# Kernel tuning notes

Measured on AMD Instinct MI355X. Metric: run time of the kernel, lower is better.

The kernel has to match this reference:

```python
import jax, jax.numpy as jnp
import numpy as np

INPUT_DIM = 512
NUM_CLASSES = 1000


def setup_inputs() -> dict:
    key = jax.random.key(0)
    kx, kw, kb = jax.random.split(key, 3)
    x = jax.random.normal(kx, (16384, INPUT_DIM), dtype=jnp.float32)
    # Stacked per-class Linear(input_dim, 2) params: W [C, 2, D], b [C, 2]
    lim = 1.0 / np.sqrt(INPUT_DIM)
    W = jax.random.uniform(kw, (NUM_CLASSES, 2, INPUT_DIM), dtype=jnp.float32, minval=-lim, maxval=lim)
    b = jax.random.uniform(kb, (NUM_CLASSES, 2), dtype=jnp.float32, minval=-lim, maxval=lim)
    return {"x": x, "W": W, "b": b}


def reference(x, W, b):
    # logits[b, c, t] = x[b, :] @ W[c, t, :] + b[c, t]
    logits = jnp.einsum("bd,ctd->bct", x, W) + b[None, :, :]  # [B, C, 2]
    # LogSoftmax over the 2 logits per class (torch dim=1 of the [B,2] slice)
    return jax.nn.log_softmax(logits, axis=-1)
```

## Files before the change

### kernel.cpp

```cpp
#include <hip/hip_runtime.h>
#include <cstdint>
#include <cstddef>

typedef unsigned short u16;
typedef unsigned int u32;
typedef __bf16 bf16x8 __attribute__((ext_vector_type(8)));
typedef float f32x4 __attribute__((ext_vector_type(4)));
typedef float f32x2 __attribute__((ext_vector_type(2)));
typedef u32 u32x4 __attribute__((ext_vector_type(4)));

#define M_TOT 16384
#define C_TOT 1000
#define N_PAD 1024
#define K_TOT 512
#define OUT_STRIDE 2000
#define BM 128
#define BN 128
#define BK 32
#define NT 16
#define NWG 1024

__device__ __forceinline__ u16 f2bf(float f) {
  u32 u = __float_as_uint(f);
  u = (u + 0x7FFFu + ((u >> 16) & 1u)) >> 16;
  return (u16)u;
}

__device__ __forceinline__ u32 cvtpk(float lo, float hi) {
  u32 d;
  asm("v_cvt_pk_bf16_f32 %0, %1, %2" : "=v"(d) : "v"(lo), "v"(hi));
  return d;
}

__global__ __launch_bounds__(256) void wprep_kernel(const float* __restrict__ W,
                                                    const float* __restrict__ b,
                                                    u16* __restrict__ wd,
                                                    float* __restrict__ bd) {
  const int i = blockIdx.x * 256 + threadIdx.x;
  const int c = i >> 6;
  const int seg = i & 63;
  ushort4 r0 = {0, 0, 0, 0}, r1 = {0, 0, 0, 0};
  if (c < C_TOT) {
    const float4* w0 = (const float4*)(W + (size_t)(2 * c) * K_TOT) + seg * 2;
    const float4* w1 = (const float4*)(W + (size_t)(2 * c + 1) * K_TOT) + seg * 2;
    float4 a0 = w0[0], a1 = w0[1], c0 = w1[0], c1 = w1[1];
    r0.x = f2bf(a0.x - c0.x); r0.y = f2bf(a0.y - c0.y);
    r0.z = f2bf(a0.z - c0.z); r0.w = f2bf(a0.w - c0.w);
    r1.x = f2bf(a1.x - c1.x); r1.y = f2bf(a1.y - c1.y);
    r1.z = f2bf(a1.z - c1.z); r1.w = f2bf(a1.w - c1.w);
    if (seg == 0) bd[c] = b[2 * c] - b[2 * c + 1];
  } else if (seg == 0) {
    bd[c] = 0.0f;
  }
  ushort4* d = (ushort4*)(wd + (size_t)c * K_TOT);
  d[seg * 2] = r0;
  d[seg * 2 + 1] = r1;
}

__device__ __forceinline__ void gload_lds(const u16* g, u16* l) {
  __builtin_amdgcn_global_load_lds((const __attribute__((address_space(1))) u32*)g,
                                   (__attribute__((address_space(3))) u32*)l, 16, 0, 0);
}

__device__ __forceinline__ void stage8k(const u16* __restrict__ gbase,
                                        u16* lb, int tid) {
#pragma unroll
  for (int i = 0; i < 2; ++i) {
    const int g = i * 256 + tid;
    const int lrow = g >> 3;
    const int u = (g & 7) ^ (lrow & 7);
    const int r = lrow | ((u >> 2) << 6);
    const int q = u & 3;
    gload_lds(gbase + (size_t)r * K_TOT + q * 8, lb + (size_t)g * 8);
  }
}

#define VMW(N) asm volatile("s_waitcnt vmcnt(" #N ")" ::: "memory")
#define CFENCE asm volatile("" ::: "memory")

__global__ __launch_bounds__(256, 4) void gemm_ls_kernel(const float* __restrict__ Af,
                                                         const u16* __restrict__ B,
                                                         const float* __restrict__ bdiff,
                                                         float* __restrict__ out) {
  __shared__ u16 As[2][4096];
  __shared__ u16 Bs[3][4096];

  const int tid = threadIdx.x;
  const int lane = tid & 63;
  const int w = tid >> 6;
  const int wm = w >> 1;
  const int wn = w & 1;

  const int bid = blockIdx.x;
  const int wg = (bid & 7) * (NWG / 8) + (bid >> 3);
  const int m0 = (wg >> 3) * BM;
  const int n0 = (wg & 7) * BN;

  const float* gAf = Af + (size_t)m0 * K_TOT;
  const u16* gB = B + (size_t)n0 * K_TOT;

  const int lrow0 = tid >> 3;
  const int au = (tid & 7) ^ (lrow0 & 7);
  const int qA = au & 3;
  const int rA0 = lrow0 | ((au >> 2) << 6);
  const int rA1 = (32 + lrow0) | ((au >> 2) << 6);
  const f32x4* gq0 = (const f32x4*)gAf + (size_t)rA0 * 128 + qA * 2;
  const f32x4* gq1 = (const f32x4*)gAf + (size_t)rA1 * 128 + qA * 2;

  const int ar = lane & 15;
  const int kq4 = lane >> 4;
  int offA[4], offB[4];
#pragma unroll
  for (int i = 0; i < 4; ++i) {
    int r = wm * 64 + i * 16 + ar;
    offA[i] = (r & 63) * 128 + (((((r >> 6) << 2) | kq4) ^ (r & 7)) << 4);
    r = wn * 64 + i * 16 + ar;
    offB[i] = (r & 63) * 128 + (((((r >> 6) << 2) | kq4) ^ (r & 7)) << 4);
  }

  f32x4 acc[4][4] = {};
  f32x4 areg[2][4];

#define ALOAD(T)                                   \
  do {                                             \
    areg[(T) & 1][0] = gq0[(T) * 8];               \
    areg[(T) & 1][1] = gq0[(T) * 8 + 1];           \
    areg[(T) & 1][2] = gq1[(T) * 8];               \
    areg[(T) & 1][3] = gq1[(T) * 8 + 1];           \
  } while (0)

#define ACVT_WR(T)                                                        \
  do {                                                                    \
    u32x4 w0, w1;                                                         \
    w0.x = cvtpk(areg[(T) & 1][0].x, areg[(T) & 1][0].y);                 \
    w0.y = cvtpk(areg[(T) & 1][0].z, areg[(T) & 1][0].w);                 \
    w0.z = cvtpk(areg[(T) & 1][1].x, areg[(T) & 1][1].y);                 \
    w0.w = cvtpk(areg[(T) & 1][1].z, areg[(T) & 1][1].w);                 \
    w1.x = cvtpk(areg[(T) & 1][2].x, areg[(T) & 1][2].y);                 \
    w1.y = cvtpk(areg[(T) & 1][2].z, areg[(T) & 1][2].w);                 \
    w1.z = cvtpk(areg[(T) & 1][3].x, areg[(T) & 1][3].y);                 \
    w1.w = cvtpk(areg[(T) & 1][3].z, areg[(T) & 1][3].w);                 \
    *(u32x4*)(&As[(T) & 1][(size_t)tid * 8]) = w0;                        \
    *(u32x4*)(&As[(T) & 1][(size_t)(256 + tid) * 8]) = w1;                \
  } while (0)

#define BSTAGE(T) stage8k(gB + (T) * BK, &Bs[(T) % 3][0], tid)

#define COMPUTE(T)                                                          \
  do {                                                                      \
    bf16x8 af[4], bf[4];                                                    \
    _Pragma("unroll") for (int i = 0; i < 4; ++i)                           \
        af[i] = *(const bf16x8*)((const char*)&As[(T) & 1][0] + offA[i]);   \
    _Pragma("unroll") for (int i = 0; i < 4; ++i)                           \
        bf[i] = *(const bf16x8*)((const char*)&Bs[(T) % 3][0] + offB[i]);   \
    _Pragma("unroll") for (int mi = 0; mi < 4; ++mi)                        \
        _Pragma("unroll") for (int ni = 0; ni < 4; ++ni)                    \
            acc[mi][ni] = __builtin_amdgcn_mfma_f32_16x16x32_bf16(          \
                af[mi], bf[ni], acc[mi][ni], 0, 0, 0);                      \
  } while (0)

#define STEP(T, VMN)                                         \
  do {                                                       \
    VMW(VMN);                                                \
    CFENCE;                                                  \
    ACVT_WR(T);                                              \
    if ((T) + 1 < NT) ALOAD((T) + 1);                        \
    asm volatile("s_waitcnt lgkmcnt(0)" ::: "memory");       \
    __builtin_amdgcn_s_barrier();                            \
    CFENCE;                                                  \
    if ((T) + 2 < NT) BSTAGE((T) + 2);                       \
    __builtin_amdgcn_s_setprio(1);                           \
    COMPUTE(T);                                              \
    __builtin_amdgcn_s_setprio(0);                           \
  } while (0)

  ALOAD(0);
  CFENCE;
  BSTAGE(0);
  BSTAGE(1);
  CFENCE;

  STEP(0, 2);   STEP(1, 2);   STEP(2, 2);   STEP(3, 2);
  STEP(4, 2);   STEP(5, 2);   STEP(6, 2);   STEP(7, 2);
  STEP(8, 2);   STEP(9, 2);   STEP(10, 2);  STEP(11, 2);
  STEP(12, 2);  STEP(13, 2);  STEP(14, 2);  STEP(15, 0);

  const int rbase = m0 + wm * 64 + (lane >> 4) * 4;
  const bool full = (n0 + BN <= C_TOT);

#pragma unroll
  for (int ni = 0; ni < 4; ++ni) {
    const int n = n0 + wn * 64 + ni * 16 + ar;
    if (full || n < C_TOT) {
      const float bd_r = bdiff[n];
#pragma unroll
      for (int mi = 0; mi < 4; ++mi) {
#pragma unroll
        for (int j = 0; j < 4; ++j) {
          const float d = acc[mi][ni][j] + bd_r;
          const float o0 = fminf(d, 0.0f) - __logf(1.0f + __expf(-fabsf(d)));
          const int row = rbase + mi * 16 + j;
          f32x2 v;
          v.x = o0;
          v.y = o0 - d;
          *(f32x2*)(out + (size_t)row * OUT_STRIDE + 2 * n) = v;
        }
      }
    }
  }
#undef ALOAD
#undef ACVT_WR
#undef BSTAGE
#undef COMPUTE
#undef STEP
}

__global__ __launch_bounds__(256) void naive_kernel(const float* __restrict__ x,
                                                    const float* __restrict__ W,
                                                    const float* __restrict__ b,
                                                    float* __restrict__ out) {
  __shared__ float xs[K_TOT];
  const int row = blockIdx.x;
  for (int i = threadIdx.x; i < K_TOT; i += 256) xs[i] = x[(size_t)row * K_TOT + i];
  __syncthreads();
  for (int c = threadIdx.x; c < C_TOT; c += 256) {
    const float* w0 = W + (size_t)c * 1024;
    float l0 = b[c * 2], l1 = b[c * 2 + 1];
    for (int k = 0; k < K_TOT; ++k) {
      const float xv = xs[k];
      l0 += xv * w0[k];
      l1 += xv * w0[K_TOT + k];
    }
    const float d = l0 - l1;
    const float t = __logf(1.0f + __expf(-fabsf(d)));
    out[(size_t)row * OUT_STRIDE + c * 2]     = fminf(d, 0.0f) - t;
    out[(size_t)row * OUT_STRIDE + c * 2 + 1] = fminf(-d, 0.0f) - t;
  }
}

extern "C" void kernel_launch(void* const* d_in, const int* in_sizes, int n_in,
                              void* d_out, int out_size, void* d_ws, size_t ws_size,
                              hipStream_t stream) {
  const float* x = (const float*)d_in[0];
  const float* W = (const float*)d_in[1];
  const float* b = (const float*)d_in[2];
  float* out = (float*)d_out;

  const size_t nwd = (size_t)N_PAD * K_TOT;
  const size_t need = nwd * sizeof(u16) + N_PAD * sizeof(float);

  if (ws_size < need) {
    naive_kernel<<<M_TOT, 256, 0, stream>>>(x, W, b, out);
    return;
  }

  u16* wd = (u16*)d_ws;
  float* bd = (float*)(wd + nwd);

  wprep_kernel<<<256, 256, 0, stream>>>(W, b, wd, bd);
  gemm_ls_kernel<<<NWG, 256, 0, stream>>>(x, wd, bd, out);
}
```

Before: 48.78 us.

## Process two M tiles per workgroup and overlap first epilogue with second tile's loads

Halves the grid so each workgroup computes two consecutive 128-row tiles against the same B column block. The second tile's A and B prefetches are issued before the first tile's log-softmax epilogue, so the output stores and transcendental math can overlap with global loads. This cuts launch and prologue cost per tile, but halves the number of workgroups, which may reduce occupancy and wave-level parallelism across CUs.

```diff
diff --git a/kernel.cpp b/kernel.cpp
--- a/kernel.cpp
+++ b/kernel.cpp
@@ -18,7 +18,7 @@
 #define BN 128
 #define BK 32
 #define NT 16
-#define NWG 1024
+#define NWG 512
 
 __device__ __forceinline__ u16 f2bf(float f) {
   u32 u = __float_as_uint(f);
@@ -93,10 +93,10 @@
 
   const int bid = blockIdx.x;
   const int wg = (bid & 7) * (NWG / 8) + (bid >> 3);
-  const int m0 = (wg >> 3) * BM;
+  const int m_base = (wg >> 3) * (2 * BM);
   const int n0 = (wg & 7) * BN;
 
-  const float* gAf = Af + (size_t)m0 * K_TOT;
+  const float* gAf = Af + (size_t)m_base * K_TOT;
   const u16* gB = B + (size_t)n0 * K_TOT;
 
   const int lrow0 = tid >> 3;
@@ -120,13 +120,14 @@
 
   f32x4 acc[4][4] = {};
   f32x4 areg[2][4];
-
-#define ALOAD(T)                                   \
-  do {                                             \
-    areg[(T) & 1][0] = gq0[(T) * 8];               \
-    areg[(T) & 1][1] = gq0[(T) * 8 + 1];           \
-    areg[(T) & 1][2] = gq1[(T) * 8];               \
-    areg[(T) & 1][3] = gq1[(T) * 8 + 1];           \
+  const bool full = (n0 + BN <= C_TOT);
+
+#define ALOAD(TOFF, T)                                   \
+  do {                                                   \
+    areg[(T) & 1][0] = gq0[(TOFF) + (T) * 8];            \
+    areg[(T) & 1][1] = gq0[(TOFF) + (T) * 8 + 1];        \
+    areg[(T) & 1][2] = gq1[(TOFF) + (T) * 8];            \
+    areg[(T) & 1][3] = gq1[(TOFF) + (T) * 8 + 1];        \
   } while (0)
 
 #define ACVT_WR(T)                                                        \
@@ -159,12 +160,12 @@
                 af[mi], bf[ni], acc[mi][ni], 0, 0, 0);                      \
   } while (0)
 
-#define STEP(T, VMN)                                         \
+#define STEP(TOFF, T, VMN)                                   \
   do {                                                       \
     VMW(VMN);                                                \
     CFENCE;                                                  \
     ACVT_WR(T);                                              \
-    if ((T) + 1 < NT) ALOAD((T) + 1);                        \
+    if ((T) + 1 < NT) ALOAD(TOFF, (T) + 1);                  \
     asm volatile("s_waitcnt lgkmcnt(0)" ::: "memory");       \
     __builtin_amdgcn_s_barrier();                            \
     CFENCE;                                                  \
@@ -174,45 +175,68 @@
     __builtin_amdgcn_s_setprio(0);                           \
   } while (0)
 
-  ALOAD(0);
+#define EPI(M0V)                                                            \
+  do {                                                                      \
+    const int rbase = (M0V) + wm * 64 + (lane >> 4) * 4;                    \
+    _Pragma("unroll") for (int ni = 0; ni < 4; ++ni) {                      \
+      const int n = n0 + wn * 64 + ni * 16 + ar;                            \
+      if (full || n < C_TOT) {                                              \
+        const float bd_r = bdiff[n];                                        \
+        _Pragma("unroll") for (int mi = 0; mi < 4; ++mi) {                  \
+          _Pragma("unroll") for (int j = 0; j < 4; ++j) {                   \
+            const float d = acc[mi][ni][j] + bd_r;                          \
+            const float o0 = fminf(d, 0.0f) - __logf(1.0f + __expf(-fabsf(d))); \
+            const int row = rbase + mi * 16 + j;                            \
+            f32x2 v;                                                        \
+            v.x = o0;                                                       \
+            v.y = o0 - d;                                                   \
+            *(f32x2*)(out + (size_t)row * OUT_STRIDE + 2 * n) = v;          \
+          }                                                                 \
+        }                                                                   \
+      }                                                                     \
+    }                                                                       \
+  } while (0)
+
+  ALOAD(0, 0);
   CFENCE;
   BSTAGE(0);
   BSTAGE(1);
   CFENCE;
 
-  STEP(0, 2);   STEP(1, 2);   STEP(2, 2);   STEP(3, 2);
-  STEP(4, 2);   STEP(5, 2);   STEP(6, 2);   STEP(7, 2);
-  STEP(8, 2);   STEP(9, 2);   STEP(10, 2);  STEP(11, 2);
-  STEP(12, 2);  STEP(13, 2);  STEP(14, 2);  STEP(15, 0);
-
-  const int rbase = m0 + wm * 64 + (lane >> 4) * 4;
-  const bool full = (n0 + BN <= C_TOT);
-
-#pragma unroll
-  for (int ni = 0; ni < 4; ++ni) {
-    const int n = n0 + wn * 64 + ni * 16 + ar;
-    if (full || n < C_TOT) {
-      const float bd_r = bdiff[n];
-#pragma unroll
-      for (int mi = 0; mi < 4; ++mi) {
-#pragma unroll
-        for (int j = 0; j < 4; ++j) {
-          const float d = acc[mi][ni][j] + bd_r;
-          const float o0 = fminf(d, 0.0f) - __logf(1.0f + __expf(-fabsf(d)));
-          const int row = rbase + mi * 16 + j;
-          f32x2 v;
-          v.x = o0;
-          v.y = o0 - d;
-          *(f32x2*)(out + (size_t)row * OUT_STRIDE + 2 * n) = v;
-        }
-      }
-    }
-  }
+  STEP(0, 0, 2);   STEP(0, 1, 2);   STEP(0, 2, 2);   STEP(0, 3, 2);
+  STEP(0, 4, 2);   STEP(0, 5, 2);   STEP(0, 6, 2);   STEP(0, 7, 2);
+  STEP(0, 8, 2);   STEP(0, 9, 2);   STEP(0, 10, 2);  STEP(0, 11, 2);
+  STEP(0, 12, 2);  STEP(0, 13, 2);  STEP(0, 14, 2);  STEP(0, 15, 0);
+
+  __builtin_amdgcn_s_barrier();
+  CFENCE;
+  ALOAD(16384, 0);
+  BSTAGE(0);
+  BSTAGE(1);
+  CFENCE;
+  EPI(m_base);
+  CFENCE;
+
+#pragma unroll
+  for (int mi = 0; mi < 4; ++mi)
+#pragma unroll
+    for (int ni = 0; ni < 4; ++ni)
+#pragma unroll
+      for (int j = 0; j < 4; ++j) acc[mi][ni][j] = 0.0f;
+
+  STEP(16384, 0, 2);   STEP(16384, 1, 2);   STEP(16384, 2, 2);   STEP(16384, 3, 2);
+  STEP(16384, 4, 2);   STEP(16384, 5, 2);   STEP(16384, 6, 2);   STEP(16384, 7, 2);
+  STEP(16384, 8, 2);   STEP(16384, 9, 2);   STEP(16384, 10, 2);  STEP(16384, 11, 2);
+  STEP(16384, 12, 2);  STEP(16384, 13, 2);  STEP(16384, 14, 2);  STEP(16384, 15, 0);
+
+  EPI(m_base + BM);
+
 #undef ALOAD
 #undef ACVT_WR
 #undef BSTAGE
 #undef COMPUTE
 #undef STEP
+#undef EPI
 }
 
 __global__ __launch_bounds__(256) void naive_kernel(const float* __restrict__ x,
```

Result: slower. 77.77 us (+59.4%).

## Process two M tiles per block and overlap first tile's epilogue with second GEMM

Applied to the files above, without the earlier changes.

Halves BN to 64 and has each workgroup compute two consecutive 128-row M tiles. The first tile's biased logits are packed to bf16 in registers and their log-softmax stores are interleaved into the second tile's main loop, hiding output-write latency behind MFMA work. This cuts accumulator registers per tile, but it reduces B reuse per A load and rounds the first tile's logits to bf16 before the epilogue, which lowers output precision.

```diff
diff --git a/kernel.cpp b/kernel.cpp
--- a/kernel.cpp
+++ b/kernel.cpp
@@ -15,7 +15,7 @@
 #define K_TOT 512
 #define OUT_STRIDE 2000
 #define BM 128
-#define BN 128
+#define BN 64
 #define BK 32
 #define NT 16
 #define NWG 1024
@@ -62,17 +62,11 @@
                                    (__attribute__((address_space(3))) u32*)l, 16, 0, 0);
 }
 
-__device__ __forceinline__ void stage8k(const u16* __restrict__ gbase,
+__device__ __forceinline__ void stage4k(const u16* __restrict__ gbase,
                                         u16* lb, int tid) {
-#pragma unroll
-  for (int i = 0; i < 2; ++i) {
-    const int g = i * 256 + tid;
-    const int lrow = g >> 3;
-    const int u = (g & 7) ^ (lrow & 7);
-    const int r = lrow | ((u >> 2) << 6);
-    const int q = u & 3;
-    gload_lds(gbase + (size_t)r * K_TOT + q * 8, lb + (size_t)g * 8);
-  }
+  const int r = tid >> 2;
+  const int q = (tid & 3) ^ (r & 3);
+  gload_lds(gbase + (size_t)r * K_TOT + q * 8, lb + (size_t)tid * 8);
 }
 
 #define VMW(N) asm volatile("s_waitcnt vmcnt(" #N ")" ::: "memory")
@@ -83,7 +77,7 @@
                                                          const float* __restrict__ bdiff,
                                                          float* __restrict__ out) {
   __shared__ u16 As[2][4096];
-  __shared__ u16 Bs[3][4096];
+  __shared__ u16 Bs[3][2048];
 
   const int tid = threadIdx.x;
   const int lane = tid & 63;
@@ -93,10 +87,10 @@
 
   const int bid = blockIdx.x;
   const int wg = (bid & 7) * (NWG / 8) + (bid >> 3);
-  const int m0 = (wg >> 3) * BM;
-  const int n0 = (wg & 7) * BN;
-
-  const float* gAf = Af + (size_t)m0 * K_TOT;
+  const int m_base = (wg >> 4) * (2 * BM);
+  const int n0 = (wg & 15) * BN;
+
+  const float* gAf = Af + (size_t)m_base * K_TOT;
   const u16* gB = B + (size_t)n0 * K_TOT;
 
   const int lrow0 = tid >> 3;
@@ -109,24 +103,32 @@
 
   const int ar = lane & 15;
   const int kq4 = lane >> 4;
-  int offA[4], offB[4];
+  int offA[4], offB[2];
 #pragma unroll
   for (int i = 0; i < 4; ++i) {
-    int r = wm * 64 + i * 16 + ar;
+    const int r = wm * 64 + i * 16 + ar;
     offA[i] = (r & 63) * 128 + (((((r >> 6) << 2) | kq4) ^ (r & 7)) << 4);
-    r = wn * 64 + i * 16 + ar;
-    offB[i] = (r & 63) * 128 + (((((r >> 6) << 2) | kq4) ^ (r & 7)) << 4);
-  }
-
-  f32x4 acc[4][4] = {};
+  }
+#pragma unroll
+  for (int i = 0; i < 2; ++i) {
+    const int r = wn * 32 + i * 16 + ar;
+    offB[i] = r * 64 + ((kq4 ^ (r & 3)) << 4);
+  }
+
+  const bool full = (n0 + BN <= C_TOT);
+  const float bd0 = bdiff[n0 + wn * 32 + ar];
+  const float bd1 = bdiff[n0 + wn * 32 + 16 + ar];
+  CFENCE;
+
+  f32x4 acc[4][2] = {};
   f32x4 areg[2][4];
 
-#define ALOAD(T)                                   \
-  do {                                             \
-    areg[(T) & 1][0] = gq0[(T) * 8];               \
-    areg[(T) & 1][1] = gq0[(T) * 8 + 1];           \
-    areg[(T) & 1][2] = gq1[(T) * 8];               \
-    areg[(T) & 1][3] = gq1[(T) * 8 + 1];           \
+#define ALOAD(TOFF, T)                                   \
+  do {                                                   \
+    areg[(T) & 1][0] = gq0[(TOFF) + (T) * 8];            \
+    areg[(T) & 1][1] = gq0[(TOFF) + (T) * 8 + 1];        \
+    areg[(T) & 1][2] = gq1[(TOFF) + (T) * 8];            \
+    areg[(T) & 1][3] = gq1[(TOFF) + (T) * 8 + 1];        \
   } while (0)
 
 #define ACVT_WR(T)                                                        \
@@ -144,27 +146,43 @@
     *(u32x4*)(&As[(T) & 1][(size_t)(256 + tid) * 8]) = w1;                \
   } while (0)
 
-#define BSTAGE(T) stage8k(gB + (T) * BK, &Bs[(T) % 3][0], tid)
+#define BSTAGE(T) stage4k(gB + (T) * BK, &Bs[(T) % 3][0], tid)
 
 #define COMPUTE(T)                                                          \
   do {                                                                      \
-    bf16x8 af[4], bf[4];                                                    \
+    bf16x8 af[4], bf[2];                                                    \
     _Pragma("unroll") for (int i = 0; i < 4; ++i)                           \
         af[i] = *(const bf16x8*)((const char*)&As[(T) & 1][0] + offA[i]);   \
-    _Pragma("unroll") for (int i = 0; i < 4; ++i)                           \
+    _Pragma("unroll") for (int i = 0; i < 2; ++i)                           \
         bf[i] = *(const bf16x8*)((const char*)&Bs[(T) % 3][0] + offB[i]);   \
     _Pragma("unroll") for (int mi = 0; mi < 4; ++mi)                        \
-        _Pragma("unroll") for (int ni = 0; ni < 4; ++ni)                    \
+        _Pragma("unroll") for (int ni = 0; ni < 2; ++ni)                    \
             acc[mi][ni] = __builtin_amdgcn_mfma_f32_16x16x32_bf16(          \
                 af[mi], bf[ni], acc[mi][ni], 0, 0, 0);                      \
   } while (0)
 
-#define STEP(T, VMN)                                         \
+#define STONE(K)                                                            \
+  do {                                                                      \
+    const int ni_ = (K) >> 4, mi_ = ((K) >> 2) & 3, j_ = (K) & 3;           \
+    const int n_ = n0 + wn * 32 + ni_ * 16 + ar;                            \
+    if (full || n_ < C_TOT) {                                               \
+      const u32 w_ = dsv[ni_ * 8 + mi_ * 2 + (j_ >> 1)];                    \
+      const float d_ = __uint_as_float((j_ & 1) ? (w_ & 0xffff0000u) : (w_ << 16)); \
+      const float o0 = fminf(d_, 0.0f) - __logf(1.0f + __expf(-fabsf(d_))); \
+      const int row = m_base + wm * 64 + mi_ * 16 + (lane >> 4) * 4 + j_;   \
+      f32x2 v_;                                                             \
+      v_.x = o0;                                                            \
+      v_.y = o0 - d_;                                                       \
+      *(f32x2*)(out + (size_t)row * OUT_STRIDE + 2 * n_) = v_;              \
+    }                                                                       \
+  } while (0)
+
+#define STEP0(T, VMN)                                        \
   do {                                                       \
     VMW(VMN);                                                \
     CFENCE;                                                  \
     ACVT_WR(T);                                              \
-    if ((T) + 1 < NT) ALOAD((T) + 1);                        \
+    if ((T) + 1 < NT) ALOAD(0, (T) + 1);                     \
     asm volatile("s_waitcnt lgkmcnt(0)" ::: "memory");       \
     __builtin_amdgcn_s_barrier();                            \
     CFENCE;                                                  \
@@ -174,32 +192,79 @@
     __builtin_amdgcn_s_setprio(0);                           \
   } while (0)
 
-  ALOAD(0);
+#define STEP1(T, VMN)                                        \
+  do {                                                       \
+    VMW(VMN);                                                \
+    CFENCE;                                                  \
+    ACVT_WR(T);                                              \
+    if ((T) + 1 < NT) ALOAD(16384, (T) + 1);                 \
+    asm volatile("s_waitcnt lgkmcnt(0)" ::: "memory");       \
+    __builtin_amdgcn_s_barrier();                            \
+    CFENCE;                                                  \
+    if ((T) + 2 < NT) BSTAGE((T) + 2);                       \
+    STONE(2 * (T));                                          \
+    STONE(2 * (T) + 1);                                      \
+    __builtin_amdgcn_s_setprio(1);                           \
+    COMPUTE(T);                                              \
+    __builtin_amdgcn_s_setprio(0);                           \
+  } while (0)
+
+  ALOAD(0, 0);
   CFENCE;
   BSTAGE(0);
   BSTAGE(1);
   CFENCE;
 
-  STEP(0, 2);   STEP(1, 2);   STEP(2, 2);   STEP(3, 2);
-  STEP(4, 2);   STEP(5, 2);   STEP(6, 2);   STEP(7, 2);
-  STEP(8, 2);   STEP(9, 2);   STEP(10, 2);  STEP(11, 2);
-  STEP(12, 2);  STEP(13, 2);  STEP(14, 2);  STEP(15, 0);
-
-  const int rbase = m0 + wm * 64 + (lane >> 4) * 4;
-  const bool full = (n0 + BN <= C_TOT);
-
-#pragma unroll
-  for (int ni = 0; ni < 4; ++ni) {
-    const int n = n0 + wn * 64 + ni * 16 + ar;
+  STEP0(0, 1);   STEP0(1, 1);   STEP0(2, 1);   STEP0(3, 1);
+  STEP0(4, 1);   STEP0(5, 1);   STEP0(6, 1);   STEP0(7, 1);
+  STEP0(8, 1);   STEP0(9, 1);   STEP0(10, 1);  STEP0(11, 1);
+  STEP0(12, 1);  STEP0(13, 1);  STEP0(14, 1);  STEP0(15, 0);
+
+  u32 dsv[16];
+#pragma unroll
+  for (int ni = 0; ni < 2; ++ni) {
+    const float bd_r = ni ? bd1 : bd0;
+#pragma unroll
+    for (int mi = 0; mi < 4; ++mi)
+#pragma unroll
+      for (int jp = 0; jp < 2; ++jp)
+        dsv[ni * 8 + mi * 2 + jp] =
+            cvtpk(acc[mi][ni][2 * jp] + bd_r, acc[mi][ni][2 * jp + 1] + bd_r);
+  }
+#pragma unroll
+  for (int mi = 0; mi < 4; ++mi)
+#pragma unroll
+    for (int ni = 0; ni < 2; ++ni)
+#pragma unroll
+      for (int j = 0; j < 4; ++j) acc[mi][ni][j] = 0.0f;
+
+  ALOAD(16384, 0);
+  CFENCE;
+  asm volatile("s_waitcnt lgkmcnt(0)" ::: "memory");
+  __builtin_amdgcn_sched_barrier(0);
+  __builtin_amdgcn_s_barrier();
+  CFENCE;
+  BSTAGE(0);
+  BSTAGE(1);
+  CFENCE;
+
+  STEP1(0, 1);   STEP1(1, 3);   STEP1(2, 3);   STEP1(3, 3);
+  STEP1(4, 3);   STEP1(5, 3);   STEP1(6, 3);   STEP1(7, 3);
+  STEP1(8, 3);   STEP1(9, 3);   STEP1(10, 3);  STEP1(11, 3);
+  STEP1(12, 3);  STEP1(13, 3);  STEP1(14, 3);  STEP1(15, 2);
+
+#pragma unroll
+  for (int ni = 0; ni < 2; ++ni) {
+    const int n = n0 + wn * 32 + ni * 16 + ar;
     if (full || n < C_TOT) {
-      const float bd_r = bdiff[n];
+      const float bd_r = ni ? bd1 : bd0;
 #pragma unroll
       for (int mi = 0; mi < 4; ++mi) {
 #pragma unroll
         for (int j = 0; j < 4; ++j) {
           const float d = acc[mi][ni][j] + bd_r;
           const float o0 = fminf(d, 0.0f) - __logf(1.0f + __expf(-fabsf(d)));
-          const int row = rbase + mi * 16 + j;
+          const int row = m_base + BM + wm * 64 + mi * 16 + (lane >> 4) * 4 + j;
           f32x2 v;
           v.x = o0;
           v.y = o0 - d;
@@ -212,7 +277,9 @@
 #undef ACVT_WR
 #undef BSTAGE
 #undef COMPUTE
-#undef STEP
+#undef STONE
+#undef STEP0
+#undef STEP1
 }
 
 __global__ __launch_bounds__(256) void naive_kernel(const float* __restrict__ x,
```

Result: slower. 52.66 us (+8.0%).
